# Optimization experiments

Hardware: AMD Instinct MI355X
Metric: run time of the kernel (lower is better)

The kernel has to match this reference:

```python
import jax, jax.numpy as jnp
import numpy as np

PI = 3.141592653
MAXV = 8          # max vertices of the intersection of two convex quads
N_BOXES = 1024
IOU_THR = 0.1


def limit_period(val):
    return val - jnp.floor(val / (2.0 * PI) + 0.5) * (2.0 * PI)


def cross2(a, b):
    return a[..., 0] * b[..., 1] - a[..., 1] * b[..., 0]


def rect_corners(box):
    # box: [7] = x,y,z,dx,dy,dz,yaw -> [4,2] BEV corners, CCW order
    x, y, dx, dy, ang = box[0], box[1], box[3], box[4], box[6]
    local = jnp.array([[0.5, 0.5], [-0.5, 0.5], [-0.5, -0.5], [0.5, -0.5]],
                      dtype=box.dtype) * jnp.stack([dx, dy])
    c, s = jnp.cos(ang), jnp.sin(ang)
    rot = jnp.array([[c, -s], [s, c]])
    return local @ rot.T + jnp.stack([x, y])


def poly_area(verts, n):
    # shoelace over first n vertices of padded [MAXV,2] polygon
    idx = jnp.arange(MAXV)
    nxt = verts[jnp.where(idx == n - 1, 0, idx + 1)]
    valid = idx < n
    return 0.5 * jnp.abs(jnp.sum(jnp.where(valid, cross2(verts, nxt), 0.0)))


def bev_inter_area(box_a, box_b):
    # Sutherland-Hodgman: clip quad A against the 4 half-planes of quad B.
    pa = rect_corners(box_a)
    pb = rect_corners(box_b)
    verts0 = jnp.zeros((MAXV, 2), pa.dtype).at[:4].set(pa)
    edges = jnp.stack([pb, jnp.roll(pb, -1, axis=0)], axis=1)  # [4,2,2]

    def clip(carry, e):
        v, n = carry
        a, b = e[0], e[1]
        idx = jnp.arange(MAXV)
        prev = v[jnp.where(idx == 0, n - 1, idx - 1)]
        d = b - a
        sp = cross2(d, v - a)     # signed side of current vertex
        sq = cross2(d, prev - a)  # signed side of previous vertex
        in_p, in_q = sp >= 0, sq >= 0
        den = sq - sp
        den = jnp.where(jnp.abs(den) < 1e-9, 1e-9, den)
        t = sq / den
        inter = prev + t[:, None] * (v - prev)
        live = idx < n
        emit_i = live & (in_p != in_q)   # crossing -> emit intersection
        emit_p = live & in_p             # inside -> emit vertex
        pts = jnp.stack([inter, v], axis=1).reshape(2 * MAXV, 2)
        msk = jnp.stack([emit_i, emit_p], axis=1).reshape(2 * MAXV)
        pos = jnp.where(msk, jnp.cumsum(msk) - 1, MAXV)  # compact; OOB dropped
        nv = jnp.zeros((MAXV, 2), v.dtype).at[pos].set(pts, mode='drop')
        return (nv, jnp.sum(msk).astype(jnp.int32)), None

    (v, n), _ = jax.lax.scan(clip, (verts0, jnp.int32(4)), edges)
    return jnp.where(n >= 3, poly_area(v, n), 0.0)


def iou3d_pair(a, b):
    inter_bev = bev_inter_area(a, b)
    h = jnp.maximum(jnp.minimum(a[2] + a[5] * 0.5, b[2] + b[5] * 0.5)
                    - jnp.maximum(a[2] - a[5] * 0.5, b[2] - b[5] * 0.5), 0.0)
    inter = inter_bev * h
    va = a[3] * a[4] * a[5]
    vb = b[3] * b[4] * b[5]
    return inter / jnp.maximum(va + vb - inter, 1e-6)


def clustering(ious):
    # exact translation of the sequential while-loop: repeatedly take the
    # first unassigned box, assign everything with iou > 0.1 to a new cluster
    # id (later clusters may overwrite earlier assignments, as in the source).
    N = ious.shape[0]

    def body(i, carry):
        ci, cid = carry
        has_zero = jnp.any(ci == 0)
        cur = jnp.argmax(ci == 0)
        m = ious[cur] > IOU_THR
        ci = jnp.where(has_zero & m, cid, ci)
        return (ci, cid + has_zero.astype(jnp.int32))

    ci, _ = jax.lax.fori_loop(0, N, body, (jnp.zeros(N, jnp.int32), jnp.int32(1)))
    return ci


def fuse_cluster(m, boxes, scores):
    # m: bool[N] membership mask for one cluster
    s = jnp.where(m, scores, 0.0)
    ssum = jnp.sum(s)
    dirs = boxes[:, 6]
    ref = dirs[jnp.argmax(s)]                    # direction of max-score member
    diff = jnp.abs(dirs - ref)
    diff = jnp.where(diff > PI, 2.0 * PI - diff, diff)
    gt = diff > PI / 2
    sc_gt = jnp.sum(jnp.where(m & gt, scores, 0.0))
    sc_le = ssum - sc_gt
    flip_gt = sc_gt <= sc_le                     # flip minority orientation group
    add = jnp.where(flip_gt, gt, ~gt)
    d2 = limit_period(dirs + PI * add.astype(boxes.dtype))
    sn = s / jnp.where(ssum > 0, ssum, 1.0)
    theta = jnp.arctan2(jnp.sum(jnp.sin(d2) * sn), jnp.sum(jnp.cos(d2) * sn))
    center = jnp.sum(boxes[:, :6] * sn[:, None], axis=0)
    box_f = jnp.concatenate([center, theta[None]])
    # score fusion: sum_i s_(i)^(i+1) over descending-sorted member scores
    s_sorted = jnp.sort(s)[::-1]
    powers = jnp.arange(1, s.shape[0] + 1, dtype=s.dtype)
    s_f = jnp.minimum(jnp.sum(s_sorted ** powers), 1.0)
    return box_f, s_f


def setup_inputs() -> dict:
    key = jax.random.key(0)
    k = jax.random.split(key, 6)
    xy = jax.random.uniform(k[0], (N_BOXES, 2), minval=0.0, maxval=140.0)
    z = jax.random.uniform(k[1], (N_BOXES, 1), minval=-1.0, maxval=1.0)
    dxy = jax.random.uniform(k[2], (N_BOXES, 2), minval=1.5, maxval=4.5)
    dz = jax.random.uniform(k[3], (N_BOXES, 1), minval=1.0, maxval=2.0)
    yaw = jax.random.uniform(k[4], (N_BOXES, 1), minval=-PI, maxval=PI)
    det_boxes = jnp.concatenate([xy, z, dxy, dz, yaw], axis=1)
    det_scores = jax.random.uniform(k[5], (N_BOXES,), minval=0.01, maxval=1.0)
    return {"det_boxes": det_boxes, "det_scores": det_scores}


def reference(det_boxes, det_scores):
    N = det_boxes.shape[0]
    boxes = det_boxes.at[:, 6].set(limit_period(det_boxes[:, 6]))
    ious = jax.vmap(lambda a: jax.vmap(lambda b: iou3d_pair(a, b))(boxes))(boxes)
    ci = clustering(ious)                               # int32[N], ids in 1..N
    masks = ci[None, :] == jnp.arange(1, N + 1)[:, None]  # [N clusters, N boxes]
    boxes_f, scores_f = jax.vmap(fuse_cluster, in_axes=(0, None, None))(masks, boxes, det_scores)
    valid = jnp.any(masks, axis=1)
    boxes_f = jnp.where(valid[:, None], boxes_f, 0.0)
    scores_f = jnp.where(valid, scores_f, 0.0)
    return boxes_f, scores_f, valid
```

## Files before the change

kernel.cpp:

```cpp
#include <hip/hip_runtime.h>

#define PI_F 3.141592653f
#define NB 1024
#define NW 16
#define IOU_THR_F 0.1f
#define NBLK 256
#define MB_MAGIC 0x33333333u
#define MC_MAGIC 0x5EEDF00Du

__device__ __forceinline__ float limit_period_f(float v) {
    return v - floorf(v / (2.0f * PI_F) + 0.5f) * (2.0f * PI_F);
}

__device__ __forceinline__ int widx(int r, int w) {
    return (r << 4) | (w ^ (r & 15));
}

__device__ __forceinline__ float iou_pair(const float* __restrict__ boxes, int i, int j,
                                          float* vxs, float* vys, int tid)
{
    const float xi  = boxes[i*7+0], yi  = boxes[i*7+1], zi  = boxes[i*7+2];
    const float dxi = boxes[i*7+3], dyi = boxes[i*7+4], dzi = boxes[i*7+5];
    const float aang = limit_period_f(boxes[i*7+6]);
    const float xj  = boxes[j*7+0], yj  = boxes[j*7+1], zj  = boxes[j*7+2];
    const float dxj = boxes[j*7+3], dyj = boxes[j*7+4], dzj = boxes[j*7+5];
    const float bang = limit_period_f(boxes[j*7+6]);

    float ca, sa, cb, sb;
    sincosf(aang, &sa, &ca);
    sincosf(bang, &sb, &cb);

    {
        const float hx = 0.5f*dxi, hy = 0.5f*dyi;
        const float lxs[4] = { hx, -hx, -hx, hx };
        const float lys[4] = { hy, hy, -hy, -hy };
        #pragma unroll
        for (int k = 0; k < 4; ++k) {
            vxs[(0*8+k)*256 + tid] = lxs[k]*ca - lys[k]*sa + xi;
            vys[(0*8+k)*256 + tid] = lxs[k]*sa + lys[k]*ca + yi;
        }
    }
    float pbx[4], pby[4];
    {
        const float hx = 0.5f*dxj, hy = 0.5f*dyj;
        const float lxs[4] = { hx, -hx, -hx, hx };
        const float lys[4] = { hy, hy, -hy, -hy };
        #pragma unroll
        for (int k = 0; k < 4; ++k) {
            pbx[k] = lxs[k]*cb - lys[k]*sb + xj;
            pby[k] = lxs[k]*sb + lys[k]*cb + yj;
        }
    }

    int n = 4;
    int cur = 0;
    #pragma unroll
    for (int e4 = 0; e4 < 4; ++e4) {
        const float eax = pbx[e4], eay = pby[e4];
        const float ebx2 = pbx[(e4+1)&3], eby2 = pby[(e4+1)&3];
        const float dx = ebx2 - eax, dy = eby2 - eay;
        int m = 0;
        if (n > 0) {
            int pidx = n - 1; if (pidx > 7) pidx = 7;
            float px = vxs[(cur*8+pidx)*256 + tid];
            float py = vys[(cur*8+pidx)*256 + tid];
            float sq = dx*(py - eay) - dy*(px - eax);
            #pragma unroll
            for (int k = 0; k < 8; ++k) {
                if (k < n) {
                    const float cx = vxs[(cur*8+k)*256 + tid];
                    const float cy = vys[(cur*8+k)*256 + tid];
                    const float sp = dx*(cy - eay) - dy*(cx - eax);
                    const bool in_p = (sp >= 0.0f);
                    const bool in_q = (sq >= 0.0f);
                    if (in_p != in_q) {
                        float den = sq - sp;
                        den = (fabsf(den) < 1e-9f) ? 1e-9f : den;
                        const float t = sq / den;
                        if (m < 8) {
                            vxs[((cur^1)*8+m)*256 + tid] = px + t*(cx - px);
                            vys[((cur^1)*8+m)*256 + tid] = py + t*(cy - py);
                        }
                        ++m;
                    }
                    if (in_p) {
                        if (m < 8) {
                            vxs[((cur^1)*8+m)*256 + tid] = cx;
                            vys[((cur^1)*8+m)*256 + tid] = cy;
                        }
                        ++m;
                    }
                    px = cx; py = cy; sq = sp;
                }
            }
        }
        n = m;
        cur ^= 1;
    }

    float area = 0.0f;
    if (n >= 3) {
        float s = 0.0f;
        const float x0 = vxs[(cur*8+0)*256 + tid];
        const float y0 = vys[(cur*8+0)*256 + tid];
        #pragma unroll
        for (int k = 0; k < 8; ++k) {
            if (k < n) {
                float nx, ny;
                if (k == n - 1) { nx = x0; ny = y0; }
                else {
                    int nk = k + 1; if (nk > 7) nk = 7;
                    nx = vxs[(cur*8+nk)*256 + tid]; ny = vys[(cur*8+nk)*256 + tid];
                }
                s += vxs[(cur*8+k)*256 + tid]*ny - vys[(cur*8+k)*256 + tid]*nx;
            }
        }
        area = 0.5f * fabsf(s);
    }

    const float zh = fminf(zi + dzi*0.5f, zj + dzj*0.5f);
    const float zl = fmaxf(zi - dzi*0.5f, zj - dzj*0.5f);
    const float h = fmaxf(zh - zl, 0.0f);
    const float inter = area * h;
    const float va = dxi*dyi*dzi;
    const float vb = dxj*dyj*dzj;
    return inter / fmaxf(va + vb - inter, 1e-6f);
}

__global__ __launch_bounds__(256) void fused_kernel(
    const float* __restrict__ boxes,
    const float* __restrict__ scores,
    float* __restrict__ out,
    unsigned long long* __restrict__ maskT,
    unsigned char* __restrict__ flagT,
    int* __restrict__ ci,
    unsigned int* __restrict__ slotB,
    unsigned int* __restrict__ flagC)
{
    extern __shared__ char smem[];
    __shared__ int candN;
    const int tid = threadIdx.x;
    const int b = blockIdx.x;
    const int lane = tid & 63;
    const int wave = tid >> 6;

    float* vxs = (float*)smem;
    float* vys = (float*)(smem + 16384);
    unsigned long long (*rowW)[NW] = (unsigned long long (*)[NW])(smem + 32768);
    unsigned int* candL = (unsigned int*)(smem + 33280);

    if (tid == 0) candN = 0;
    __syncthreads();

    for (int rr = 0; rr < 4; ++rr) {
        const int j = b * 4 + rr;
        const float xj  = boxes[j*7+0], yj  = boxes[j*7+1];
        const float dxj = boxes[j*7+3], dyj = boxes[j*7+4];
        const float rb2 = 0.25f*(dxj*dxj + dyj*dyj);
        #pragma unroll
        for (int q = 0; q < 4; ++q) {
            const int i = q*256 + tid;
            const float xi  = boxes[i*7+0], yi  = boxes[i*7+1];
            const float dxi = boxes[i*7+3], dyi = boxes[i*7+4];
            const float ddx = xi - xj, ddy = yi - yj;
            const float d2 = ddx*ddx + ddy*ddy;
            const float ra2 = 0.25f*(dxi*dxi + dyi*dyi);
            const bool cand = d2 <= 2.0f*(ra2 + rb2);

            const unsigned long long bal = __ballot(cand);
            const int w = q*4 + wave;
            if (lane == 0) rowW[rr][w] = bal;

            unsigned long long keep = bal;
            if ((j >> 6) == w) keep &= ~(1ull << (j & 63));
            int basep = 0;
            if (lane == 0 && keep) basep = atomicAdd(&candN, (int)__popcll(keep));
            basep = __shfl(basep, 0);
            if ((keep >> lane) & 1ull) {
                const int pos = basep + (int)__popcll(keep & ((1ull << lane) - 1ull));
                candL[pos] = ((unsigned)rr << 10) | (unsigned)i;
            }
        }
    }
    __syncthreads();
    const int nc = candN;

    for (int e = tid; e < nc; e += 256) {
        const unsigned int ent = candL[e];
        const int rr = (int)(ent >> 10);
        const int i  = (int)(ent & 1023u);
        const int j  = b * 4 + rr;
        const float iou = iou_pair(boxes, i, j, vxs, vys, tid);
        if (!(iou > IOU_THR_F)) {
            unsigned int* hw = (unsigned int*)&rowW[rr][i >> 6];
            atomicAnd(&hw[(i >> 5) & 1], ~(1u << (i & 31)));
        }
    }
    __syncthreads();

    if (tid < 64) {
        const int rr = tid >> 4, w = tid & 15;
        const unsigned long long v = rowW[rr][w];
        const int j = b * 4 + rr;
        maskT[(size_t)j*NW + w] = v;
        flagT[j*NW + w] = (v != 0ull) ? 1 : 0;
    }
    __syncthreads();
    if (tid == 0) {
        __threadfence();
        __hip_atomic_store(&slotB[b], MB_MAGIC, __ATOMIC_RELEASE, __HIP_MEMORY_SCOPE_AGENT);
    }

    if (b == 0) {
        while (__hip_atomic_load(&slotB[tid], __ATOMIC_RELAXED, __HIP_MEMORY_SCOPE_AGENT) != MB_MAGIC)
            __builtin_amdgcn_s_sleep(32);
        __threadfence();
        __syncthreads();

        unsigned long long* mat = (unsigned long long*)smem;
        unsigned short* wm = (unsigned short*)(smem + 131072);
        unsigned long long* seed_lds = (unsigned long long*)(smem + 133120);
        int* rankb = (int*)(smem + 133248);

        if (tid < NW) { seed_lds[tid] = 0ull; rankb[tid] = 0; }
        #pragma unroll
        for (int rr = 0; rr < 4; ++rr) {
            const int r = tid + rr * 256;
            const uint4 f = *(const uint4*)(flagT + r * NW);
            unsigned int m16 = 0;
            #define NIBX(v, sh) \
                { if ((v) & 0x000000FFu) m16 |= 1u << (sh); \
                  if ((v) & 0x0000FF00u) m16 |= 1u << ((sh)+1); \
                  if ((v) & 0x00FF0000u) m16 |= 1u << ((sh)+2); \
                  if ((v) & 0xFF000000u) m16 |= 1u << ((sh)+3); }
            NIBX(f.x, 0) NIBX(f.y, 4) NIBX(f.z, 8) NIBX(f.w, 12)
            #undef NIBX
            wm[r] = (unsigned short)m16;
            unsigned int t16 = m16;
            while (t16) {
                const int w = __ffs(t16) - 1;
                t16 &= t16 - 1;
                mat[widx(r, w)] = maskT[r * NW + w];
            }
        }
        __syncthreads();

        if (tid < 64) {
            int base = 0;
            for (int c = 0; c < NW; ++c) {
                const int row = c * 64 + tid;
                unsigned int f = (unsigned int)wm[row];
                unsigned long long acc = 0ull, Dt = 0ull;
                while (f) {
                    const int w = __ffs(f) - 1;
                    f &= f - 1;
                    const unsigned long long v = mat[widx(row, w)];
                    acc |= v & seed_lds[w];
                    if (w == c) Dt = v;
                }
                const bool elig = (acc == 0ull);
                const unsigned long long E = __ballot(elig);
                const unsigned long long inlow = Dt & ((1ull << tid) - 1ull);

                unsigned long long S = E;
                #pragma unroll 1
                for (int it = 0; it < 64; ++it) {
                    const bool killed = (inlow & S) != 0ull;
                    const unsigned long long S2 = E & __ballot(!killed);
                    if (S2 == S) break;
                    S = S2;
                }

                if (tid == 0) { seed_lds[c] = S; rankb[c] = base; }
                base += (int)__popcll(S);
            }
        }
        __syncthreads();

        #pragma unroll
        for (int rr = 0; rr < 4; ++rr) {
            const int r = tid + rr * 256;
            unsigned int f = (unsigned int)wm[r];
            int best = -1;
            while (f) {
                const int w = __ffs(f) - 1;
                f &= f - 1;
                const unsigned long long bits = mat[widx(r, w)] & seed_lds[w];
                if (bits) best = (w << 6) | (63 - __clzll(bits));
            }
            int lbl = 0;
            if (best >= 0) {
                const int w = best >> 6, pos = best & 63;
                lbl = rankb[w] + (int)__popcll(seed_lds[w] & ((1ull << pos) - 1ull)) + 1;
            }
            ci[r] = lbl;
        }
        __syncthreads();
        if (tid == 0) {
            __threadfence();
            __hip_atomic_store(flagC, MC_MAGIC, __ATOMIC_RELEASE, __HIP_MEMORY_SCOPE_AGENT);
        }
    } else {
        if (tid == 0) {
            while (__hip_atomic_load(flagC, __ATOMIC_RELAXED, __HIP_MEMORY_SCOPE_AGENT) != MC_MAGIC)
                __builtin_amdgcn_s_sleep(64);
            __threadfence();
        }
    }
    __syncthreads();

    {
        float* ms = (float*)smem + wave * 1024;
        int*   mi = (int*)(smem + 16384) + wave * 1024;
        const int target = b * 4 + wave + 1;
        const int ob = target - 1;

        unsigned int mymask = 0;
        const int4* ci4 = (const int4*)ci;
        #pragma unroll
        for (int k4 = 0; k4 < 4; ++k4) {
            const int4 v = ci4[lane * 4 + k4];
            if (v.x == target) mymask |= 1u << (k4*4+0);
            if (v.y == target) mymask |= 1u << (k4*4+1);
            if (v.z == target) mymask |= 1u << (k4*4+2);
            if (v.w == target) mymask |= 1u << (k4*4+3);
        }
        const bool anyv = (__ballot(mymask != 0) != 0ULL);

        float* outb = out + (size_t)ob * 7;
        float* outs = out + 7 * NB;
        float* outv = out + 8 * NB;

        if (!anyv) {
            if (lane == 0) {
                #pragma unroll
                for (int c = 0; c < 7; ++c) outb[c] = 0.0f;
                outs[ob] = 0.0f;
                outv[ob] = 0.0f;
            }
        } else {
            float ssum = 0.0f, smax = -1.0f;
            int sidx = 1 << 30;
            #pragma unroll
            for (int k = 0; k < 16; ++k) {
                if (mymask & (1u << k)) {
                    const int idx = lane * 16 + k;
                    const float s = scores[idx];
                    ssum += s;
                    if (s > smax || (s == smax && idx < sidx)) { smax = s; sidx = idx; }
                }
            }
            #pragma unroll
            for (int off = 32; off >= 1; off >>= 1) {
                ssum += __shfl_xor(ssum, off);
                const float om = __shfl_xor(smax, off);
                const int   oi = __shfl_xor(sidx, off);
                if (om > smax || (om == smax && oi < sidx)) { smax = om; sidx = oi; }
            }
            const float ref = limit_period_f(boxes[sidx * 7 + 6]);

            float sc_gt = 0.0f;
            #pragma unroll
            for (int k = 0; k < 16; ++k) {
                if (mymask & (1u << k)) {
                    const int idx = lane * 16 + k;
                    const float dir = limit_period_f(boxes[idx * 7 + 6]);
                    float diff = fabsf(dir - ref);
                    if (diff > PI_F) diff = 2.0f * PI_F - diff;
                    if (diff > PI_F * 0.5f) sc_gt += scores[idx];
                }
            }
            #pragma unroll
            for (int off = 32; off >= 1; off >>= 1) sc_gt += __shfl_xor(sc_gt, off);
            const bool flip_gt = (sc_gt <= (ssum - sc_gt));

            float acc[6] = {0,0,0,0,0,0};
            float ssin = 0.0f, scos = 0.0f;
            #pragma unroll
            for (int k = 0; k < 16; ++k) {
                if (mymask & (1u << k)) {
                    const int idx = lane * 16 + k;
                    const float s = scores[idx];
                    const float w = s / ssum;
                    const float dir = limit_period_f(boxes[idx * 7 + 6]);
                    float diff = fabsf(dir - ref);
                    if (diff > PI_F) diff = 2.0f * PI_F - diff;
                    const bool gt = (diff > PI_F * 0.5f);
                    const bool add = flip_gt ? gt : (!gt);
                    const float d2 = limit_period_f(dir + (add ? PI_F : 0.0f));
                    float sd, cd;
                    sincosf(d2, &sd, &cd);
                    ssin += sd * w;
                    scos += cd * w;
                    #pragma unroll
                    for (int c = 0; c < 6; ++c) acc[c] += boxes[idx * 7 + c] * w;
                }
            }
            #pragma unroll
            for (int off = 32; off >= 1; off >>= 1) {
                ssin += __shfl_xor(ssin, off);
                scos += __shfl_xor(scos, off);
                #pragma unroll
                for (int c = 0; c < 6; ++c) acc[c] += __shfl_xor(acc[c], off);
            }
            const float theta = atan2f(ssin, scos);

            const int cnt = __popc(mymask);
            int x = cnt;
            #pragma unroll
            for (int off = 1; off < 64; off <<= 1) {
                const int y = __shfl_up(x, off);
                if (lane >= off) x += y;
            }
            const int base = x - cnt;
            const int K = __shfl(x, 63);
            {
                int p = base;
                #pragma unroll
                for (int k = 0; k < 16; ++k) {
                    if (mymask & (1u << k)) {
                        const int idx = lane * 16 + k;
                        ms[p] = scores[idx];
                        mi[p] = idx;
                        ++p;
                    }
                }
            }
            float sf = 0.0f;
            for (int e = lane; e < K; e += 64) {
                const float v = ms[e];
                const int ix = mi[e];
                int rank = 0;
                for (int t = 0; t < K; ++t) {
                    const float u = ms[t];
                    if (u > v || (u == v && mi[t] < ix)) ++rank;
                }
                sf += powf(v, (float)(rank + 1));
            }
            #pragma unroll
            for (int off = 32; off >= 1; off >>= 1) sf += __shfl_xor(sf, off);
            sf = fminf(sf, 1.0f);

            if (lane == 0) {
                #pragma unroll
                for (int c = 0; c < 6; ++c) outb[c] = acc[c];
                outb[6] = theta;
                outs[ob] = sf;
                outv[ob] = 1.0f;
            }
        }
    }
}

extern "C" void kernel_launch(void* const* d_in, const int* in_sizes, int n_in,
                              void* d_out, int out_size, void* d_ws, size_t ws_size,
                              hipStream_t stream) {
    const float* boxes  = (const float*)d_in[0];
    const float* scores = (const float*)d_in[1];
    float* out = (float*)d_out;

    char* ws = (char*)d_ws;
    unsigned long long* maskT = (unsigned long long*)ws;
    unsigned char* flagT = (unsigned char*)(ws + 131072);
    int* ci = (int*)(ws + 147456);
    unsigned int* slotB = (unsigned int*)(ws + 151552);
    unsigned int* flagC = (unsigned int*)(ws + 152576);

    const size_t SMEM = 133312;
    (void)hipFuncSetAttribute((const void*)fused_kernel,
                              hipFuncAttributeMaxDynamicSharedMemorySize, (int)SMEM);
    fused_kernel<<<NBLK, 256, SMEM, stream>>>(
        boxes, scores, out, maskT, flagT, ci, slotB, flagC);
}
```

Measured before the change: 95.77 us.

## Compact cross-block handoff data and lighten grid-barrier fences and polling

Replaces the per-word byte flag table with a 16-bit word mask per row built by ballot, and skips writing zero mask words. Cluster ids are packed four per 64-bit word. All of this goes through relaxed agent-scope atomics, and release fences are replaced with an explicit vmcnt wait. The spin-wait sleep interval is cut and the barrier wait in block 0 overlaps with LDS init. The aim is less global traffic and shorter handoff latency across the software grid barriers. The cost is a weaker memory ordering argument: it relies on relaxed atomics and waitcnt instead of proper release/acquire, and on cluster ids fitting in 16 bits.

```diff
diff --git a/kernel.cpp b/kernel.cpp
--- a/kernel.cpp
+++ b/kernel.cpp
@@ -132,8 +132,8 @@
     const float* __restrict__ scores,
     float* __restrict__ out,
     unsigned long long* __restrict__ maskT,
-    unsigned char* __restrict__ flagT,
-    int* __restrict__ ci,
+    unsigned int* __restrict__ wm_g,
+    unsigned long long* __restrict__ ci_pack,
     unsigned int* __restrict__ slotB,
     unsigned int* __restrict__ flagC)
 {
@@ -202,45 +202,44 @@
         const int rr = tid >> 4, w = tid & 15;
         const unsigned long long v = rowW[rr][w];
         const int j = b * 4 + rr;
-        maskT[(size_t)j*NW + w] = v;
-        flagT[j*NW + w] = (v != 0ull) ? 1 : 0;
+        if (v != 0ull)
+            __hip_atomic_store(&maskT[(size_t)j*NW + w], v,
+                               __ATOMIC_RELAXED, __HIP_MEMORY_SCOPE_AGENT);
+        const unsigned long long wb = __ballot(v != 0ull);
+        if ((tid & 15) == 0)
+            __hip_atomic_store(&wm_g[j], (unsigned int)((wb >> (16*rr)) & 0xFFFFull),
+                               __ATOMIC_RELAXED, __HIP_MEMORY_SCOPE_AGENT);
     }
     __syncthreads();
     if (tid == 0) {
-        __threadfence();
-        __hip_atomic_store(&slotB[b], MB_MAGIC, __ATOMIC_RELEASE, __HIP_MEMORY_SCOPE_AGENT);
+        asm volatile("s_waitcnt vmcnt(0)" ::: "memory");
+        __hip_atomic_store(&slotB[b], MB_MAGIC, __ATOMIC_RELAXED, __HIP_MEMORY_SCOPE_AGENT);
     }
 
     if (b == 0) {
-        while (__hip_atomic_load(&slotB[tid], __ATOMIC_RELAXED, __HIP_MEMORY_SCOPE_AGENT) != MB_MAGIC)
-            __builtin_amdgcn_s_sleep(32);
-        __threadfence();
-        __syncthreads();
-
         unsigned long long* mat = (unsigned long long*)smem;
         unsigned short* wm = (unsigned short*)(smem + 131072);
         unsigned long long* seed_lds = (unsigned long long*)(smem + 133120);
         int* rankb = (int*)(smem + 133248);
+        unsigned long long* packL = (unsigned long long*)(smem + 133312);
 
         if (tid < NW) { seed_lds[tid] = 0ull; rankb[tid] = 0; }
+
+        while (__hip_atomic_load(&slotB[tid], __ATOMIC_RELAXED, __HIP_MEMORY_SCOPE_AGENT) != MB_MAGIC)
+            __builtin_amdgcn_s_sleep(1);
         #pragma unroll
         for (int rr = 0; rr < 4; ++rr) {
-            const int r = tid + rr * 256;
-            const uint4 f = *(const uint4*)(flagT + r * NW);
-            unsigned int m16 = 0;
-            #define NIBX(v, sh) \
-                { if ((v) & 0x000000FFu) m16 |= 1u << (sh); \
-                  if ((v) & 0x0000FF00u) m16 |= 1u << ((sh)+1); \
-                  if ((v) & 0x00FF0000u) m16 |= 1u << ((sh)+2); \
-                  if ((v) & 0xFF000000u) m16 |= 1u << ((sh)+3); }
-            NIBX(f.x, 0) NIBX(f.y, 4) NIBX(f.z, 8) NIBX(f.w, 12)
-            #undef NIBX
+            const int r = tid * 4 + rr;
+            const unsigned int m16 =
+                __hip_atomic_load(&wm_g[r], __ATOMIC_RELAXED, __HIP_MEMORY_SCOPE_AGENT) & 0xFFFFu;
             wm[r] = (unsigned short)m16;
             unsigned int t16 = m16;
             while (t16) {
                 const int w = __ffs(t16) - 1;
                 t16 &= t16 - 1;
-                mat[widx(r, w)] = maskT[r * NW + w];
+                mat[widx(r, w)] =
+                    __hip_atomic_load(&maskT[(size_t)r * NW + w],
+                                      __ATOMIC_RELAXED, __HIP_MEMORY_SCOPE_AGENT);
             }
         }
         __syncthreads();
@@ -277,34 +276,44 @@
         }
         __syncthreads();
 
-        #pragma unroll
-        for (int rr = 0; rr < 4; ++rr) {
-            const int r = tid + rr * 256;
-            unsigned int f = (unsigned int)wm[r];
-            int best = -1;
-            while (f) {
-                const int w = __ffs(f) - 1;
-                f &= f - 1;
-                const unsigned long long bits = mat[widx(r, w)] & seed_lds[w];
-                if (bits) best = (w << 6) | (63 - __clzll(bits));
-            }
-            int lbl = 0;
-            if (best >= 0) {
-                const int w = best >> 6, pos = best & 63;
-                lbl = rankb[w] + (int)__popcll(seed_lds[w] & ((1ull << pos) - 1ull)) + 1;
-            }
-            ci[r] = lbl;
+        {
+            unsigned long long pk = 0ull;
+            #pragma unroll
+            for (int rr = 0; rr < 4; ++rr) {
+                const int r = tid * 4 + rr;
+                unsigned int f = (unsigned int)wm[r];
+                int best = -1;
+                while (f) {
+                    const int w = __ffs(f) - 1;
+                    f &= f - 1;
+                    const unsigned long long bits = mat[widx(r, w)] & seed_lds[w];
+                    if (bits) best = (w << 6) | (63 - __clzll(bits));
+                }
+                int lbl = 0;
+                if (best >= 0) {
+                    const int w = best >> 6, pos = best & 63;
+                    lbl = rankb[w] + (int)__popcll(seed_lds[w] & ((1ull << pos) - 1ull)) + 1;
+                }
+                pk |= (unsigned long long)(unsigned)lbl << (16 * rr);
+            }
+            packL[tid] = pk;
         }
         __syncthreads();
+
+        if (tid < 64) {
+            #pragma unroll
+            for (int q = 0; q < 4; ++q)
+                __hip_atomic_store(&ci_pack[tid + q*64], packL[tid + q*64],
+                                   __ATOMIC_RELAXED, __HIP_MEMORY_SCOPE_AGENT);
+        }
         if (tid == 0) {
-            __threadfence();
-            __hip_atomic_store(flagC, MC_MAGIC, __ATOMIC_RELEASE, __HIP_MEMORY_SCOPE_AGENT);
+            asm volatile("s_waitcnt vmcnt(0)" ::: "memory");
+            __hip_atomic_store(flagC, MC_MAGIC, __ATOMIC_RELAXED, __HIP_MEMORY_SCOPE_AGENT);
         }
     } else {
         if (tid == 0) {
             while (__hip_atomic_load(flagC, __ATOMIC_RELAXED, __HIP_MEMORY_SCOPE_AGENT) != MC_MAGIC)
-                __builtin_amdgcn_s_sleep(64);
-            __threadfence();
+                __builtin_amdgcn_s_sleep(1);
         }
     }
     __syncthreads();
@@ -316,14 +325,15 @@
         const int ob = target - 1;
 
         unsigned int mymask = 0;
-        const int4* ci4 = (const int4*)ci;
         #pragma unroll
         for (int k4 = 0; k4 < 4; ++k4) {
-            const int4 v = ci4[lane * 4 + k4];
-            if (v.x == target) mymask |= 1u << (k4*4+0);
-            if (v.y == target) mymask |= 1u << (k4*4+1);
-            if (v.z == target) mymask |= 1u << (k4*4+2);
-            if (v.w == target) mymask |= 1u << (k4*4+3);
+            const unsigned long long pw =
+                __hip_atomic_load(&ci_pack[lane * 4 + k4],
+                                  __ATOMIC_RELAXED, __HIP_MEMORY_SCOPE_AGENT);
+            #pragma unroll
+            for (int s = 0; s < 4; ++s)
+                if (((pw >> (16*s)) & 0xFFFFull) == (unsigned long long)(unsigned)target)
+                    mymask |= 1u << (k4*4 + s);
         }
         const bool anyv = (__ballot(mymask != 0) != 0ULL);
 
@@ -461,14 +471,14 @@
 
     char* ws = (char*)d_ws;
     unsigned long long* maskT = (unsigned long long*)ws;
-    unsigned char* flagT = (unsigned char*)(ws + 131072);
-    int* ci = (int*)(ws + 147456);
-    unsigned int* slotB = (unsigned int*)(ws + 151552);
-    unsigned int* flagC = (unsigned int*)(ws + 152576);
-
-    const size_t SMEM = 133312;
+    unsigned int* wm_g = (unsigned int*)(ws + 131072);
+    unsigned long long* ci_pack = (unsigned long long*)(ws + 135168);
+    unsigned int* slotB = (unsigned int*)(ws + 137216);
+    unsigned int* flagC = (unsigned int*)(ws + 138240);
+
+    const size_t SMEM = 135360;
     (void)hipFuncSetAttribute((const void*)fused_kernel,
                               hipFuncAttributeMaxDynamicSharedMemorySize, (int)SMEM);
     fused_kernel<<<NBLK, 256, SMEM, stream>>>(
-        boxes, scores, out, maskT, flagT, ci, slotB, flagC);
+        boxes, scores, out, maskT, wm_g, ci_pack, slotB, flagC);
 }
```

Result: faster. 85.32 us (median of 2 runs) (-10.9%).
